# Kernel tuning notes

Hardware: AMD Instinct MI355X
Metric: run time of the kernel (lower is better)

## Reference

```python
import jax, jax.numpy as jnp
import numpy as np

TEMP = 0.07
EPS = 1e-6
NORM_EPS = 1e-12  # F.normalize default eps
LN_EPS = 1e-5

B, D, H, W = 32, 256, 64, 64
K = 256
DFF = 2048


def _l2norm(v, axis):
    n = jnp.sqrt(jnp.sum(v * v, axis=axis, keepdims=True))
    return v / jnp.maximum(n, NORM_EPS)


def _layernorm(v, g, b):
    mu = jnp.mean(v, axis=-1, keepdims=True)
    var = jnp.mean((v - mu) ** 2, axis=-1, keepdims=True)
    return (v - mu) * jax.lax.rsqrt(var + LN_EPS) * g + b


def setup_inputs() -> dict:
    key = jax.random.key(0)
    ks = jax.random.split(key, 8)
    s1 = 1.0 / np.sqrt(D)
    s2 = 1.0 / np.sqrt(DFF)
    return {
        "x": jax.random.normal(ks[0], (B, D, H, W), jnp.float32),
        "tgt": jax.random.normal(ks[1], (B, K, D), jnp.float32),
        "w1": jax.random.uniform(ks[2], (DFF, D), jnp.float32, -s1, s1),
        "b1": jax.random.uniform(ks[3], (DFF,), jnp.float32, -s1, s1),
        "w2": jax.random.uniform(ks[4], (D, DFF), jnp.float32, -s2, s2),
        "b2": jax.random.uniform(ks[5], (D,), jnp.float32, -s2, s2),
        "g2": jnp.ones((D,), jnp.float32),
        "be2": jnp.zeros((D,), jnp.float32),
        "g3": jnp.ones((D,), jnp.float32),
        "be3": jnp.zeros((D,), jnp.float32),
    }


def reference(x, tgt, w1, b1, w2, b2, g2, be2, g3, be3):
    # slot cross-attention with L2-normalized q/k
    tn = _l2norm(tgt, axis=2)           # (b,k,d)
    xn = _l2norm(x, axis=1)             # (b,d,h,w)
    dots = jnp.einsum('bkd,bdhw->bkhw', tn, xn)
    attn = jax.nn.softmax(dots / TEMP, axis=1) + EPS          # softmax over slots
    attn = attn / jnp.sum(attn, axis=(2, 3), keepdims=True)   # spatial normalization
    tgt2 = jnp.einsum('bdhw,bkhw->bkd', x, attn)
    t = _layernorm(tgt + tgt2, g2, be2)
    # FFN (dropout = identity in eval)
    ff = jnp.maximum(t @ w1.T + b1, 0.0) @ w2.T + b2
    return _layernorm(t + ff, g3, be3)
```

## Files before the change

### kernel.cpp

```cpp
#include <hip/hip_runtime.h>
#include <hip/hip_bf16.h>

using bf16 = __hip_bfloat16;

typedef __attribute__((ext_vector_type(8))) short short8;
typedef __attribute__((ext_vector_type(4))) float f32x4;

constexpr int Bb = 32, Dd = 256, HWw = 4096, Kk = 256, Ff = 2048;
constexpr float TEMP_INV = 1.0f / 0.07f;
constexpr float EPSf = 1e-6f;
constexpr float NORM_EPSf = 1e-12f;
constexpr float LN_EPSf = 1e-5f;
constexpr size_t PKD = (size_t)Bb * Kk * Dd;

static __device__ __forceinline__ float b2f(bf16 v) { return __bfloat162float(v); }
static __device__ __forceinline__ bf16 f2b(float v) { return __float2bfloat16(v); }


__global__ __launch_bounds__(64) void k_tn(const float* __restrict__ tgt,
                                           bf16* __restrict__ tnbf) {
  int row = blockIdx.x;
  int b = row >> 8, slot = row & 255;
  int lane = threadIdx.x;
  const float* src = tgt + (size_t)row * Dd + lane * 4;
  float v[4];
#pragma unroll
  for (int u = 0; u < 4; u++) v[u] = src[u];
  float ss = v[0] * v[0] + v[1] * v[1] + v[2] * v[2] + v[3] * v[3];
#pragma unroll
  for (int m = 32; m >= 1; m >>= 1) ss += __shfl_xor(ss, m, 64);
  float inv = 1.0f / fmaxf(sqrtf(ss), NORM_EPSf);
  bf16 o[4] __attribute__((aligned(8)));
#pragma unroll
  for (int u = 0; u < 4; u++) o[u] = f2b(v[u] * inv);
  int s = lane >> 3;
  int q2 = (lane >> 1) & 3;
  int jh = (lane & 1) * 4;
  size_t fi = (size_t)((slot >> 4) * 64 + q2 * 16 + (slot & 15));
  *(float2*)(tnbf + ((size_t)(b * 8 + s) * 1024 + fi) * 8 + jh) = *(float2*)o;
}

__global__ __launch_bounds__(64) void k_prew1(const float* __restrict__ w1,
                                              bf16* __restrict__ w1bf) {
  int f = blockIdx.x;
  int lane = threadIdx.x;
  const float* src = w1 + (size_t)f * Dd + lane * 4;
  bf16 o[4] __attribute__((aligned(8)));
#pragma unroll
  for (int u = 0; u < 4; u++) o[u] = f2b(src[u]);
  int s = lane >> 3;
  int q2 = (lane >> 1) & 3;
  int jh = (lane & 1) * 4;
  size_t fi = (size_t)(((f & 63) >> 4) * 64 + q2 * 16 + (f & 15));
  *(float2*)(w1bf + ((size_t)((f >> 6) * 8 + s) * 256 + fi) * 8 + jh) = *(float2*)o;
}

__global__ __launch_bounds__(64) void k_prew2(const float* __restrict__ w2,
                                              bf16* __restrict__ w2bf) {
  int d = blockIdx.x;
  int lane = threadIdx.x;
  const float* src = w2 + (size_t)d * Ff + lane * 32;
  size_t gbase = (size_t)((d >> 6) * 64 + lane) * 256;
  int fbase = ((d & 63) >> 4) * 64 + (d & 15);
#pragma unroll
  for (int q2 = 0; q2 < 4; q2++) {
    float4 v0 = *(const float4*)(src + q2 * 8);
    float4 v1 = *(const float4*)(src + q2 * 8 + 4);
    bf16 o[8] __attribute__((aligned(16)));
    o[0] = f2b(v0.x); o[1] = f2b(v0.y); o[2] = f2b(v0.z); o[3] = f2b(v0.w);
    o[4] = f2b(v1.x); o[5] = f2b(v1.y); o[6] = f2b(v1.z); o[7] = f2b(v1.w);
    *(float4*)(w2bf + (gbase + fbase + q2 * 16) * 8) = *(float4*)o;
  }
}

#define MFMA16(a, b, c) __builtin_amdgcn_mfma_f32_16x16x32_bf16(a, b, c, 0, 0, 0)

__global__ __launch_bounds__(256) void k_dots(const bf16* __restrict__ tnbf,
                                              const float* __restrict__ x,
                                              bf16* __restrict__ xb_bf,
                                              bf16* __restrict__ attn_bf,
                                              float* __restrict__ S) {
  __shared__ __align__(16) char smem[16384];
  bf16* Bs = (bf16*)smem;
  float* ssred = (float*)(smem + 8320);
  float* nxl = (float*)(smem + 12672);
  float* red = (float*)(smem + 12928);
  int b = blockIdx.x >> 6;
  int hw0 = (blockIdx.x & 63) * 64;
  int tid = threadIdx.x;
  int wave = tid >> 6, lane = tid & 63;
  int quad = lane >> 4, nl = lane & 15;

  int dp = tid >> 4;
  int ch = tid & 15;
  int qb = dp >> 2;
  int jb = (dp & 3) * 2;

  f32x4 acc[4][4];
#pragma unroll
  for (int i = 0; i < 4; i++)
#pragma unroll
    for (int j = 0; j < 4; j++) acc[i][j] = (f32x4){0.f, 0.f, 0.f, 0.f};
  float ssp[4] = {0.f, 0.f, 0.f, 0.f};

  int spx = (hw0 >> 5) + (ch >> 3);
  int q2x = (ch >> 1) & 3;
  int jx = (ch & 1) * 4;

  float4 va, vb;
  short8 afp[4];
  {
    const float* xr0 = x + (size_t)((b << 8) + 2 * dp) * HWw + hw0 + ch * 4;
    va = *(const float4*)xr0;
    vb = *(const float4*)(xr0 + HWw);
    const bf16* ts0 = tnbf + (size_t)(b * 8) * 1024 * 8;
#pragma unroll
    for (int mt = 0; mt < 4; mt++)
      afp[mt] = *(const short8*)(ts0 + (size_t)(((wave << 2) + mt) * 64 + lane) * 8);
  }

  for (int s = 0; s < 8; s++) {
    bf16* bsb = Bs + (s & 1) * 2080;
    {
      float vva[4] = {va.x, va.y, va.z, va.w};
      float vvb[4] = {vb.x, vb.y, vb.z, vb.w};
      bf16 pa[4] __attribute__((aligned(8)));
      bf16 pb[4] __attribute__((aligned(8)));
#pragma unroll
      for (int jj = 0; jj < 4; jj++) {
        ssp[jj] += vva[jj] * vva[jj] + vvb[jj] * vvb[jj];
        pa[jj] = f2b(vva[jj]);
        pb[jj] = f2b(vvb[jj]);
      }
      int d0r = s * 32 + 2 * dp;
      int fiA = (d0r >> 4) * 64 + q2x * 16 + (d0r & 15);
      size_t base = ((size_t)(b * 128) + spx) * 1024;
      *(float2*)(xb_bf + (base + fiA) * 8 + jx) = *(float2*)pa;
      *(float2*)(xb_bf + (base + fiA + 1) * 8 + jx) = *(float2*)pb;
#pragma unroll
      for (int jj = 0; jj < 4; jj++) {
        int hwl = ch * 4 + jj;
        int nt = hwl >> 4;
        int li = (qb << 4) | (hwl & 15);
        union { bf16 h[2]; unsigned int u; } pk;
        pk.h[0] = pa[jj];
        pk.h[1] = pb[jj];
        *(unsigned int*)&bsb[nt * 520 + li * 8 + jb] = pk.u;
      }
    }
    __syncthreads();
    short8 af[4];
#pragma unroll
    for (int mt = 0; mt < 4; mt++) af[mt] = afp[mt];
    if (s < 7) {
      const float* xr = x + (size_t)((b << 8) + (s + 1) * 32 + 2 * dp) * HWw + hw0 + ch * 4;
      va = *(const float4*)xr;
      vb = *(const float4*)(xr + HWw);
      const bf16* tsrc = tnbf + (size_t)(b * 8 + s + 1) * 1024 * 8;
#pragma unroll
      for (int mt = 0; mt < 4; mt++)
        afp[mt] = *(const short8*)(tsrc + (size_t)(((wave << 2) + mt) * 64 + lane) * 8);
    }
    short8 bfv[4];
#pragma unroll
    for (int nt = 0; nt < 4; nt++)
      bfv[nt] = *(const short8*)(bsb + nt * 520 + lane * 8);
#pragma unroll
    for (int mt = 0; mt < 4; mt++)
#pragma unroll
      for (int nt = 0; nt < 4; nt++) acc[mt][nt] = MFMA16(af[mt], bfv[nt], acc[mt][nt]);
  }

#pragma unroll
  for (int jj = 0; jj < 4; jj++) ssred[(ch * 4 + jj) * 17 + dp] = ssp[jj];
  __syncthreads();
  if (tid < 64) {
    float sum = 0.f;
#pragma unroll
    for (int i = 0; i < 16; i++) sum += ssred[tid * 17 + i];
    nxl[tid] = TEMP_INV / fmaxf(sqrtf(sum), NORM_EPSf);
  }
  __syncthreads();

  float sc[4];
#pragma unroll
  for (int nt = 0; nt < 4; nt++) sc[nt] = nxl[nt * 16 + nl];
#pragma unroll
  for (int mt = 0; mt < 4; mt++)
#pragma unroll
    for (int nt = 0; nt < 4; nt++)
#pragma unroll
      for (int r = 0; r < 4; r++) acc[mt][nt][r] *= sc[nt];

  float* red2 = red + 256;

  float pmax[4];
#pragma unroll
  for (int nt = 0; nt < 4; nt++) {
    float m = acc[0][nt][0];
#pragma unroll
    for (int mt = 0; mt < 4; mt++)
#pragma unroll
      for (int r = 0; r < 4; r++) m = fmaxf(m, acc[mt][nt][r]);
    m = fmaxf(m, __shfl_xor(m, 16, 64));
    m = fmaxf(m, __shfl_xor(m, 32, 64));
    pmax[nt] = m;
  }
  if (lane < 16) {
#pragma unroll
    for (int nt = 0; nt < 4; nt++) red[((wave << 2) + nt) * 16 + nl] = pmax[nt];
  }
  __syncthreads();
  float cmax[4];
#pragma unroll
  for (int nt = 0; nt < 4; nt++) {
    float m = red[nt * 16 + nl];
#pragma unroll
    for (int w2 = 1; w2 < 4; w2++) m = fmaxf(m, red[((w2 << 2) + nt) * 16 + nl]);
    cmax[nt] = m;
  }

  float psum[4];
#pragma unroll
  for (int nt = 0; nt < 4; nt++) {
    float s = 0.f;
#pragma unroll
    for (int mt = 0; mt < 4; mt++)
#pragma unroll
      for (int r = 0; r < 4; r++) {
        float e = __expf(acc[mt][nt][r] - cmax[nt]);
        acc[mt][nt][r] = e;
        s += e;
      }
    s += __shfl_xor(s, 16, 64);
    s += __shfl_xor(s, 32, 64);
    psum[nt] = s;
  }
  if (lane < 16) {
#pragma unroll
    for (int nt = 0; nt < 4; nt++) red2[((wave << 2) + nt) * 16 + nl] = psum[nt];
  }
  __syncthreads();
  float ci[4];
#pragma unroll
  for (int nt = 0; nt < 4; nt++) {
    float s = 0.f;
#pragma unroll
    for (int w2 = 0; w2 < 4; w2++) s += red2[((w2 << 2) + nt) * 16 + nl];
    ci[nt] = 1.0f / s;
  }

#pragma unroll
  for (int mt = 0; mt < 4; mt++) {
    int slotg = (b << 8) + (wave << 6) + (mt << 4) + (quad << 2);
#pragma unroll
    for (int r = 0; r < 4; r++) {
      float rs = 0.f;
#pragma unroll
      for (int nt = 0; nt < 4; nt++) {
        bf16 hb = f2b(acc[mt][nt][r] * ci[nt] + EPSf);
        float q = b2f(hb);
        acc[mt][nt][r] = q;
        rs += q;
      }
      rs += __shfl_xor(rs, 1, 64);
      rs += __shfl_xor(rs, 2, 64);
      rs += __shfl_xor(rs, 4, 64);
      rs += __shfl_xor(rs, 8, 64);
      if (nl == 0) atomicAdd(&S[slotg + r], rs);
    }
  }

  __syncthreads();
  bf16* rp = (bf16*)smem;
  int jat = nl & 7;
#pragma unroll
  for (int h = 0; h < 2; h++) {
#pragma unroll
    for (int mt = 0; mt < 4; mt++) {
      int fi0 = ((wave << 2) + mt) * 64 + (quad << 2);
#pragma unroll
      for (int ntl = 0; ntl < 2; ntl++) {
        int nt = (h << 1) + ntl;
        int q2p = (ntl << 1) + (nl >> 3);
#pragma unroll
        for (int r = 0; r < 4; r++)
          rp[(fi0 + q2p * 16 + r) * 8 + jat] = f2b(acc[mt][nt][r]);
      }
    }
    __syncthreads();
    size_t gbase = ((size_t)(b * 128) + (hw0 >> 5) + h) * 1024 * 8;
#pragma unroll
    for (int u = 0; u < 4; u++) {
      short8 vv = *(const short8*)(rp + u * 2048 + tid * 8);
      *(short8*)(attn_bf + gbase + u * 2048 + tid * 8) = vv;
    }
    if (h == 0) __syncthreads();
  }
}

__global__ __launch_bounds__(256) void k_gemm2(const bf16* __restrict__ attn_bf,
                                               const bf16* __restrict__ xb_bf,
                                               float* __restrict__ t2p) {
  int n = blockIdx.x;
  int b = n & 31;
  int r2 = n >> 5;
  int kp = r2 & 3;
  int dgrp = (r2 >> 2) & 3;
  int hs = r2 >> 4;
  int tid = threadIdx.x;
  int wave = tid >> 6, lane = tid & 63;
  int wr = wave >> 1, wc = wave & 1;

  f32x4 acc[2][2];
#pragma unroll
  for (int i = 0; i < 2; i++)
#pragma unroll
    for (int j = 0; j < 2; j++) acc[i][j] = (f32x4){0.f, 0.f, 0.f, 0.f};

  const bf16* Abase = attn_bf + ((size_t)(b * 128 + hs * 32) * 1024 + (size_t)(kp * 4 + wr * 2) * 64) * 8;
  const bf16* Bbase = xb_bf + ((size_t)(b * 128 + hs * 32) * 1024 + (size_t)(dgrp * 4 + wc * 2) * 64) * 8;
#pragma unroll 4
  for (int st = 0; st < 32; st++) {
    const bf16* Ap = Abase + (size_t)st * 1024 * 8;
    const bf16* Bp = Bbase + (size_t)st * 1024 * 8;
    short8 a0 = *(const short8*)(Ap + (size_t)lane * 8);
    short8 a1 = *(const short8*)(Ap + (size_t)(64 + lane) * 8);
    short8 b0 = *(const short8*)(Bp + (size_t)lane * 8);
    short8 b1 = *(const short8*)(Bp + (size_t)(64 + lane) * 8);
    acc[0][0] = MFMA16(a0, b0, acc[0][0]);
    acc[0][1] = MFMA16(a0, b1, acc[0][1]);
    acc[1][0] = MFMA16(a1, b0, acc[1][0]);
    acc[1][1] = MFMA16(a1, b1, acc[1][1]);
  }
  float* dst = t2p + (size_t)hs * PKD;
  int quad = lane >> 4, nl = lane & 15;
#pragma unroll
  for (int i = 0; i < 2; i++)
#pragma unroll
    for (int r = 0; r < 4; r++) {
      int row = (b << 8) + kp * 64 + wr * 32 + i * 16 + quad * 4 + r;
#pragma unroll
      for (int j = 0; j < 2; j++) {
        int col = dgrp * 64 + wc * 32 + j * 16 + nl;
        dst[(size_t)row * Dd + col] = acc[i][j][r];
      }
    }
}

__global__ __launch_bounds__(64) void k_ln_pre(const float* __restrict__ t2p,
                                               const float* __restrict__ S,
                                               const float* __restrict__ tgt,
                                               const float* __restrict__ g,
                                               const float* __restrict__ be,
                                               float* __restrict__ t,
                                               bf16* __restrict__ tbf) {
  int row = blockIdx.x;
  int lane = threadIdx.x;
  float sInv = 1.0f / S[row];
  size_t off = (size_t)row * Dd + lane * 4;
  float4 a0 = *(const float4*)(t2p + off);
  float4 a1 = *(const float4*)(t2p + PKD + off);
  float4 a2 = *(const float4*)(t2p + 2 * PKD + off);
  float4 a3 = *(const float4*)(t2p + 3 * PKD + off);
  const float* pt = tgt + off;
  float v[4];
  v[0] = (a0.x + a1.x + a2.x + a3.x) * sInv + pt[0];
  v[1] = (a0.y + a1.y + a2.y + a3.y) * sInv + pt[1];
  v[2] = (a0.z + a1.z + a2.z + a3.z) * sInv + pt[2];
  v[3] = (a0.w + a1.w + a2.w + a3.w) * sInv + pt[3];
  float s1 = v[0] + v[1] + v[2] + v[3];
  float s2 = v[0] * v[0] + v[1] * v[1] + v[2] * v[2] + v[3] * v[3];
#pragma unroll
  for (int m = 32; m >= 1; m >>= 1) {
    s1 += __shfl_xor(s1, m, 64);
    s2 += __shfl_xor(s2, m, 64);
  }
  float mu = s1 * (1.0f / 256.0f);
  float var = s2 * (1.0f / 256.0f) - mu * mu;
  float rs = rsqrtf(fmaxf(var, 0.f) + LN_EPSf);
  float* po = t + (size_t)row * Dd + lane * 4;
  bf16 o[4] __attribute__((aligned(8)));
#pragma unroll
  for (int u = 0; u < 4; u++) {
    float val = (v[u] - mu) * rs * g[lane * 4 + u] + be[lane * 4 + u];
    po[u] = val;
    o[u] = f2b(val);
  }
  int s = lane >> 3;
  int q2 = (lane >> 1) & 3;
  int jh = (lane & 1) * 4;
  size_t fi = (size_t)(((row & 63) >> 4) * 64 + q2 * 16 + (row & 15));
  *(float2*)(tbf + ((size_t)((row >> 6) * 8 + s) * 256 + fi) * 8 + jh) = *(float2*)o;
}

__global__ __launch_bounds__(256) void k_ffn1(const bf16* __restrict__ tbf,
                                              const bf16* __restrict__ w1bf,
                                              const float* __restrict__ b1,
                                              bf16* __restrict__ h1bf) {
  int rowgrp = blockIdx.x >> 5;
  int fgrp = blockIdx.x & 31;
  int tid = threadIdx.x;
  int wave = tid >> 6, lane = tid & 63;
  int am = (wave >> 1) * 2, bn = (wave & 1) * 2;

  f32x4 acc[2][2];
#pragma unroll
  for (int i = 0; i < 2; i++)
#pragma unroll
    for (int j = 0; j < 2; j++) acc[i][j] = (f32x4){0.f, 0.f, 0.f, 0.f};

  const bf16* Abase = tbf + (size_t)rowgrp * 8 * 256 * 8;
  const bf16* Bbase = w1bf + (size_t)fgrp * 8 * 256 * 8;
#pragma unroll
  for (int s = 0; s < 8; s++) {
    short8 af[2], bfr[2];
#pragma unroll
    for (int i = 0; i < 2; i++)
      af[i] = *(const short8*)(Abase + ((size_t)s * 256 + ((am + i) * 64 + lane)) * 8);
#pragma unroll
    for (int j = 0; j < 2; j++)
      bfr[j] = *(const short8*)(Bbase + ((size_t)s * 256 + ((bn + j) * 64 + lane)) * 8);
#pragma unroll
    for (int i = 0; i < 2; i++)
#pragma unroll
      for (int j = 0; j < 2; j++) acc[i][j] = MFMA16(af[i], bfr[j], acc[i][j]);
  }
  int quad = lane >> 4, nl = lane & 15;
  int jat = nl & 7;
#pragma unroll
  for (int j = 0; j < 2; j++) {
    int f = fgrp * 64 + (bn + j) * 16 + nl;
    float bias = b1[f];
    size_t sp = (size_t)(rowgrp * 64) + fgrp * 2 + ((bn + j) >> 1);
    int q2p = ((bn + j) & 1) * 2 + (nl >> 3);
#pragma unroll
    for (int i = 0; i < 2; i++) {
      int fiBase = (am + i) * 64 + q2p * 16 + (quad << 2);
#pragma unroll
      for (int r = 0; r < 4; r++) {
        float val = fmaxf(acc[i][j][r] + bias, 0.f);
        h1bf[(sp * 256 + fiBase + r) * 8 + jat] = f2b(val);
      }
    }
  }
}

__global__ __launch_bounds__(256) void k_ffn2(const bf16* __restrict__ h1bf,
                                              const bf16* __restrict__ w2bf,
                                              float* __restrict__ o2p) {
  int n = blockIdx.x;
  int rowgrp = n >> 3;
  int ksp = n & 7;
  int tid = threadIdx.x;
  int wave = tid >> 6, lane = tid & 63;

  f32x4 acc[4][4];
#pragma unroll
  for (int i = 0; i < 4; i++)
#pragma unroll
    for (int j = 0; j < 4; j++) acc[i][j] = (f32x4){0.f, 0.f, 0.f, 0.f};

#pragma unroll
  for (int st = 0; st < 8; st++) {
    int sg = ksp * 8 + st;
    const bf16* Ab = h1bf + ((size_t)(rowgrp * 64 + sg) * 256) * 8;
    const bf16* Bbv = w2bf + ((size_t)(wave * 64 + sg) * 256) * 8;
    short8 af[4], bfr[4];
#pragma unroll
    for (int mt = 0; mt < 4; mt++)
      af[mt] = *(const short8*)(Ab + (size_t)(mt * 64 + lane) * 8);
#pragma unroll
    for (int nt = 0; nt < 4; nt++)
      bfr[nt] = *(const short8*)(Bbv + (size_t)(nt * 64 + lane) * 8);
#pragma unroll
    for (int mt = 0; mt < 4; mt++)
#pragma unroll
      for (int nt = 0; nt < 4; nt++) acc[mt][nt] = MFMA16(af[mt], bfr[nt], acc[mt][nt]);
  }
  float* dst = o2p + (size_t)ksp * PKD;
  int quad = lane >> 4, nl = lane & 15;
#pragma unroll
  for (int mt = 0; mt < 4; mt++)
#pragma unroll
    for (int r = 0; r < 4; r++) {
      int row = rowgrp * 64 + mt * 16 + quad * 4 + r;
#pragma unroll
      for (int nt = 0; nt < 4; nt++) {
        int col = wave * 64 + nt * 16 + nl;
        dst[(size_t)row * Dd + col] = acc[mt][nt][r];
      }
    }
}

__global__ __launch_bounds__(64) void k_ln_out(const float* __restrict__ o2p,
                                               const float* __restrict__ b2v,
                                               const float* __restrict__ t,
                                               const float* __restrict__ g,
                                               const float* __restrict__ be,
                                               float* __restrict__ out) {
  int row = blockIdx.x;
  int lane = threadIdx.x;
  size_t off = (size_t)row * Dd + lane * 4;
  float acc4[4] = {0.f, 0.f, 0.f, 0.f};
#pragma unroll
  for (int q = 0; q < 8; q++) {
    float4 aq = *(const float4*)(o2p + (size_t)q * PKD + off);
    acc4[0] += aq.x;
    acc4[1] += aq.y;
    acc4[2] += aq.z;
    acc4[3] += aq.w;
  }
  const float* pt = t + off;
  float v[4];
#pragma unroll
  for (int u = 0; u < 4; u++) v[u] = acc4[u] + b2v[lane * 4 + u] + pt[u];
  float s1 = v[0] + v[1] + v[2] + v[3];
  float s2 = v[0] * v[0] + v[1] * v[1] + v[2] * v[2] + v[3] * v[3];
#pragma unroll
  for (int m = 32; m >= 1; m >>= 1) {
    s1 += __shfl_xor(s1, m, 64);
    s2 += __shfl_xor(s2, m, 64);
  }
  float mu = s1 * (1.0f / 256.0f);
  float var = s2 * (1.0f / 256.0f) - mu * mu;
  float rs = rsqrtf(fmaxf(var, 0.f) + LN_EPSf);
  float* pw = out + (size_t)row * Dd + lane * 4;
#pragma unroll
  for (int u = 0; u < 4; u++)
    pw[u] = (v[u] - mu) * rs * g[lane * 4 + u] + be[lane * 4 + u];
}

extern "C" void kernel_launch(void* const* d_in, const int* in_sizes, int n_in,
                              void* d_out, int out_size, void* d_ws, size_t ws_size,
                              hipStream_t stream) {
  const float* x = (const float*)d_in[0];
  const float* tgt = (const float*)d_in[1];
  const float* w1 = (const float*)d_in[2];
  const float* b1 = (const float*)d_in[3];
  const float* w2 = (const float*)d_in[4];
  const float* b2v = (const float*)d_in[5];
  const float* g2 = (const float*)d_in[6];
  const float* be2 = (const float*)d_in[7];
  const float* g3 = (const float*)d_in[8];
  const float* be3 = (const float*)d_in[9];
  float* out = (float*)d_out;

  char* w = (char*)d_ws;
  bf16* tnbf = (bf16*)w;     w += (size_t)Bb * Kk * Dd * 2;
  float* S = (float*)w;      w += (size_t)Bb * Kk * 4;
  float* t = (float*)w;      w += (size_t)Bb * Kk * Dd * 4;
  bf16* attn_bf = (bf16*)w;  w += (size_t)Bb * HWw * Kk * 2;
  bf16* h1bf = (bf16*)w;     w += (size_t)Bb * Kk * Ff * 2;
  bf16* xb_bf = (bf16*)w;    w += (size_t)Bb * Dd * HWw * 2;

  bf16* tbf = tnbf;
  bf16* w1bf = attn_bf;
  bf16* w2bf = attn_bf + (size_t)Ff * Dd;
  float* t2p = (float*)h1bf;
  float* o2p = (float*)xb_bf;

  hipMemsetAsync(S, 0, (size_t)Bb * Kk * 4, stream);
  k_tn<<<Bb * Kk, 64, 0, stream>>>(tgt, tnbf);
  k_dots<<<Bb * (HWw / 64), 256, 0, stream>>>(tnbf, x, xb_bf, attn_bf, S);
  k_gemm2<<<2048, 256, 0, stream>>>(attn_bf, xb_bf, t2p);
  k_prew1<<<Ff, 64, 0, stream>>>(w1, w1bf);
  k_prew2<<<Dd, 64, 0, stream>>>(w2, w2bf);
  k_ln_pre<<<Bb * Kk, 64, 0, stream>>>(t2p, S, tgt, g2, be2, t, tbf);
  k_ffn1<<<(Bb * Kk / 64) * (Ff / 64), 256, 0, stream>>>(tbf, w1bf, b1, h1bf);
  k_ffn2<<<(Bb * Kk / 64) * 8, 256, 0, stream>>>(h1bf, w2bf, o2p);
  k_ln_out<<<Bb * Kk, 64, 0, stream>>>(o2p, b2v, t, g3, be3, out);
}
```

Baseline: 411.0 us.

## Remove split-K partial buffers, swizzle staged stores, move xb_bf store past barrier

k_gemm2 stops splitting the spatial reduction into four partial outputs and instead loops over the whole 4096 range per block. k_ffn2 now reduces its K-split across waves in shared memory rather than writing eight global partials. Both LN kernels therefore read a single buffer. k_dots and k_ffn1 stage their bf16 outputs through LDS with an XOR swizzle so global writes are coalesced, and the xb_bf global store in k_dots now happens after the barrier. The aim is to cut global partial-sum traffic and scattered stores, at the cost of fewer blocks (less parallelism) in gemm2 and ffn2 and more shared memory in ffn2.

```diff
diff --git a/kernel.cpp b/kernel.cpp
--- a/kernel.cpp
+++ b/kernel.cpp
@@ -11,7 +11,6 @@
 constexpr float EPSf = 1e-6f;
 constexpr float NORM_EPSf = 1e-12f;
 constexpr float LN_EPSf = 1e-5f;
-constexpr size_t PKD = (size_t)Bb * Kk * Dd;
 
 static __device__ __forceinline__ float b2f(bf16 v) { return __bfloat162float(v); }
 static __device__ __forceinline__ bf16 f2b(float v) { return __float2bfloat16(v); }
@@ -121,22 +120,17 @@
 
   for (int s = 0; s < 8; s++) {
     bf16* bsb = Bs + (s & 1) * 2080;
+    bf16 pa[4] __attribute__((aligned(8)));
+    bf16 pb[4] __attribute__((aligned(8)));
     {
       float vva[4] = {va.x, va.y, va.z, va.w};
       float vvb[4] = {vb.x, vb.y, vb.z, vb.w};
-      bf16 pa[4] __attribute__((aligned(8)));
-      bf16 pb[4] __attribute__((aligned(8)));
 #pragma unroll
       for (int jj = 0; jj < 4; jj++) {
         ssp[jj] += vva[jj] * vva[jj] + vvb[jj] * vvb[jj];
         pa[jj] = f2b(vva[jj]);
         pb[jj] = f2b(vvb[jj]);
       }
-      int d0r = s * 32 + 2 * dp;
-      int fiA = (d0r >> 4) * 64 + q2x * 16 + (d0r & 15);
-      size_t base = ((size_t)(b * 128) + spx) * 1024;
-      *(float2*)(xb_bf + (base + fiA) * 8 + jx) = *(float2*)pa;
-      *(float2*)(xb_bf + (base + fiA + 1) * 8 + jx) = *(float2*)pb;
 #pragma unroll
       for (int jj = 0; jj < 4; jj++) {
         int hwl = ch * 4 + jj;
@@ -148,10 +142,17 @@
         *(unsigned int*)&bsb[nt * 520 + li * 8 + jb] = pk.u;
       }
     }
+    short8 af[4];
+#pragma unroll
+    for (int mt = 0; mt < 4; mt++) af[mt] = afp[mt];
     __syncthreads();
-    short8 af[4];
-#pragma unroll
-    for (int mt = 0; mt < 4; mt++) af[mt] = afp[mt];
+    {
+      int d0r = s * 32 + 2 * dp;
+      int fiA = (d0r >> 4) * 64 + q2x * 16 + (d0r & 15);
+      size_t base = ((size_t)(b * 128) + spx) * 1024;
+      *(float2*)(xb_bf + (base + fiA) * 8 + jx) = *(float2*)pa;
+      *(float2*)(xb_bf + (base + fiA + 1) * 8 + jx) = *(float2*)pb;
+    }
     if (s < 7) {
       const float* xr = x + (size_t)((b << 8) + (s + 1) * 32 + 2 * dp) * HWw + hw0 + ch * 4;
       va = *(const float4*)xr;
@@ -284,16 +285,21 @@
         int nt = (h << 1) + ntl;
         int q2p = (ntl << 1) + (nl >> 3);
 #pragma unroll
-        for (int r = 0; r < 4; r++)
-          rp[(fi0 + q2p * 16 + r) * 8 + jat] = f2b(acc[mt][nt][r]);
+        for (int r = 0; r < 4; r++) {
+          int fi = fi0 + q2p * 16 + r;
+          int fisw = fi ^ ((fi >> 3) & 3);
+          rp[fisw * 8 + jat] = f2b(acc[mt][nt][r]);
+        }
       }
     }
     __syncthreads();
     size_t gbase = ((size_t)(b * 128) + (hw0 >> 5) + h) * 1024 * 8;
 #pragma unroll
     for (int u = 0; u < 4; u++) {
-      short8 vv = *(const short8*)(rp + u * 2048 + tid * 8);
-      *(short8*)(attn_bf + gbase + u * 2048 + tid * 8) = vv;
+      int fl = u * 256 + tid;
+      int fg = fl ^ ((fl >> 3) & 3);
+      short8 vv = *(const short8*)(rp + (size_t)fl * 8);
+      *(short8*)(attn_bf + gbase + (size_t)fg * 8) = vv;
     }
     if (h == 0) __syncthreads();
   }
@@ -301,13 +307,12 @@
 
 __global__ __launch_bounds__(256) void k_gemm2(const bf16* __restrict__ attn_bf,
                                                const bf16* __restrict__ xb_bf,
-                                               float* __restrict__ t2p) {
+                                               float* __restrict__ t2) {
   int n = blockIdx.x;
   int b = n & 31;
   int r2 = n >> 5;
   int kp = r2 & 3;
-  int dgrp = (r2 >> 2) & 3;
-  int hs = r2 >> 4;
+  int dgrp = r2 >> 2;
   int tid = threadIdx.x;
   int wave = tid >> 6, lane = tid & 63;
   int wr = wave >> 1, wc = wave & 1;
@@ -318,10 +323,10 @@
 #pragma unroll
     for (int j = 0; j < 2; j++) acc[i][j] = (f32x4){0.f, 0.f, 0.f, 0.f};
 
-  const bf16* Abase = attn_bf + ((size_t)(b * 128 + hs * 32) * 1024 + (size_t)(kp * 4 + wr * 2) * 64) * 8;
-  const bf16* Bbase = xb_bf + ((size_t)(b * 128 + hs * 32) * 1024 + (size_t)(dgrp * 4 + wc * 2) * 64) * 8;
+  const bf16* Abase = attn_bf + ((size_t)(b * 128) * 1024 + (size_t)(kp * 4 + wr * 2) * 64) * 8;
+  const bf16* Bbase = xb_bf + ((size_t)(b * 128) * 1024 + (size_t)(dgrp * 4 + wc * 2) * 64) * 8;
 #pragma unroll 4
-  for (int st = 0; st < 32; st++) {
+  for (int st = 0; st < 128; st++) {
     const bf16* Ap = Abase + (size_t)st * 1024 * 8;
     const bf16* Bp = Bbase + (size_t)st * 1024 * 8;
     short8 a0 = *(const short8*)(Ap + (size_t)lane * 8);
@@ -333,7 +338,6 @@
     acc[1][0] = MFMA16(a1, b0, acc[1][0]);
     acc[1][1] = MFMA16(a1, b1, acc[1][1]);
   }
-  float* dst = t2p + (size_t)hs * PKD;
   int quad = lane >> 4, nl = lane & 15;
 #pragma unroll
   for (int i = 0; i < 2; i++)
@@ -343,12 +347,12 @@
 #pragma unroll
       for (int j = 0; j < 2; j++) {
         int col = dgrp * 64 + wc * 32 + j * 16 + nl;
-        dst[(size_t)row * Dd + col] = acc[i][j][r];
-      }
-    }
-}
-
-__global__ __launch_bounds__(64) void k_ln_pre(const float* __restrict__ t2p,
+        t2[(size_t)row * Dd + col] = acc[i][j][r];
+      }
+    }
+}
+
+__global__ __launch_bounds__(64) void k_ln_pre(const float* __restrict__ t2,
                                                const float* __restrict__ S,
                                                const float* __restrict__ tgt,
                                                const float* __restrict__ g,
@@ -359,16 +363,13 @@
   int lane = threadIdx.x;
   float sInv = 1.0f / S[row];
   size_t off = (size_t)row * Dd + lane * 4;
-  float4 a0 = *(const float4*)(t2p + off);
-  float4 a1 = *(const float4*)(t2p + PKD + off);
-  float4 a2 = *(const float4*)(t2p + 2 * PKD + off);
-  float4 a3 = *(const float4*)(t2p + 3 * PKD + off);
+  float4 a0 = *(const float4*)(t2 + off);
   const float* pt = tgt + off;
   float v[4];
-  v[0] = (a0.x + a1.x + a2.x + a3.x) * sInv + pt[0];
-  v[1] = (a0.y + a1.y + a2.y + a3.y) * sInv + pt[1];
-  v[2] = (a0.z + a1.z + a2.z + a3.z) * sInv + pt[2];
-  v[3] = (a0.w + a1.w + a2.w + a3.w) * sInv + pt[3];
+  v[0] = a0.x * sInv + pt[0];
+  v[1] = a0.y * sInv + pt[1];
+  v[2] = a0.z * sInv + pt[2];
+  v[3] = a0.w * sInv + pt[3];
   float s1 = v[0] + v[1] + v[2] + v[3];
   float s2 = v[0] * v[0] + v[1] * v[1] + v[2] * v[2] + v[3] * v[3];
 #pragma unroll
@@ -398,6 +399,7 @@
                                               const bf16* __restrict__ w1bf,
                                               const float* __restrict__ b1,
                                               bf16* __restrict__ h1bf) {
+  __shared__ __align__(16) bf16 rp[512 * 8];
   int rowgrp = blockIdx.x >> 5;
   int fgrp = blockIdx.x & 31;
   int tid = threadIdx.x;
@@ -432,7 +434,7 @@
   for (int j = 0; j < 2; j++) {
     int f = fgrp * 64 + (bn + j) * 16 + nl;
     float bias = b1[f];
-    size_t sp = (size_t)(rowgrp * 64) + fgrp * 2 + ((bn + j) >> 1);
+    int seth = (bn + j) >> 1;
     int q2p = ((bn + j) & 1) * 2 + (nl >> 3);
 #pragma unroll
     for (int i = 0; i < 2; i++) {
@@ -440,18 +442,30 @@
 #pragma unroll
       for (int r = 0; r < 4; r++) {
         float val = fmaxf(acc[i][j][r] + bias, 0.f);
-        h1bf[(sp * 256 + fiBase + r) * 8 + jat] = f2b(val);
-      }
-    }
+        int fi = fiBase + r;
+        int fisw = fi ^ ((fi >> 3) & 3);
+        rp[(seth * 256 + fisw) * 8 + jat] = f2b(val);
+      }
+    }
+  }
+  __syncthreads();
+  size_t sp0 = (size_t)(rowgrp * 64) + fgrp * 2;
+#pragma unroll
+  for (int u = 0; u < 2; u++) {
+    int loc = tid;
+    int fg = loc ^ ((loc >> 3) & 3);
+    short8 vv = *(const short8*)(rp + ((size_t)u * 256 + loc) * 8);
+    *(short8*)(h1bf + ((sp0 + u) * 256 + fg) * 8) = vv;
   }
 }
 
 __global__ __launch_bounds__(256) void k_ffn2(const bf16* __restrict__ h1bf,
                                               const bf16* __restrict__ w2bf,
-                                              float* __restrict__ o2p) {
+                                              float* __restrict__ o2) {
+  __shared__ float redsm[4 * 4160];
   int n = blockIdx.x;
-  int rowgrp = n >> 3;
-  int ksp = n & 7;
+  int rowgrp = n >> 2;
+  int cg = n & 3;
   int tid = threadIdx.x;
   int wave = tid >> 6, lane = tid & 63;
 
@@ -461,11 +475,11 @@
 #pragma unroll
     for (int j = 0; j < 4; j++) acc[i][j] = (f32x4){0.f, 0.f, 0.f, 0.f};
 
-#pragma unroll
-  for (int st = 0; st < 8; st++) {
-    int sg = ksp * 8 + st;
+#pragma unroll 4
+  for (int stl = 0; stl < 16; stl++) {
+    int sg = wave * 16 + stl;
     const bf16* Ab = h1bf + ((size_t)(rowgrp * 64 + sg) * 256) * 8;
-    const bf16* Bbv = w2bf + ((size_t)(wave * 64 + sg) * 256) * 8;
+    const bf16* Bbv = w2bf + ((size_t)(cg * 64 + sg) * 256) * 8;
     short8 af[4], bfr[4];
 #pragma unroll
     for (int mt = 0; mt < 4; mt++)
@@ -478,22 +492,29 @@
 #pragma unroll
       for (int nt = 0; nt < 4; nt++) acc[mt][nt] = MFMA16(af[mt], bfr[nt], acc[mt][nt]);
   }
-  float* dst = o2p + (size_t)ksp * PKD;
   int quad = lane >> 4, nl = lane & 15;
+  float* my = redsm + wave * 4160;
 #pragma unroll
   for (int mt = 0; mt < 4; mt++)
 #pragma unroll
     for (int r = 0; r < 4; r++) {
-      int row = rowgrp * 64 + mt * 16 + quad * 4 + r;
-#pragma unroll
-      for (int nt = 0; nt < 4; nt++) {
-        int col = wave * 64 + nt * 16 + nl;
-        dst[(size_t)row * Dd + col] = acc[mt][nt][r];
-      }
-    }
-}
-
-__global__ __launch_bounds__(64) void k_ln_out(const float* __restrict__ o2p,
+      int row = mt * 16 + quad * 4 + r;
+#pragma unroll
+      for (int nt = 0; nt < 4; nt++)
+        my[row * 65 + nt * 16 + nl] = acc[mt][nt][r];
+    }
+  __syncthreads();
+#pragma unroll
+  for (int u = 0; u < 16; u++) {
+    int o = u * 256 + tid;
+    int row = o >> 6, col = o & 63;
+    int li = row * 65 + col;
+    float ssum = redsm[li] + redsm[4160 + li] + redsm[8320 + li] + redsm[12480 + li];
+    o2[(size_t)(rowgrp * 64 + row) * Dd + cg * 64 + col] = ssum;
+  }
+}
+
+__global__ __launch_bounds__(64) void k_ln_out(const float* __restrict__ o2,
                                                const float* __restrict__ b2v,
                                                const float* __restrict__ t,
                                                const float* __restrict__ g,
@@ -502,19 +523,13 @@
   int row = blockIdx.x;
   int lane = threadIdx.x;
   size_t off = (size_t)row * Dd + lane * 4;
-  float acc4[4] = {0.f, 0.f, 0.f, 0.f};
-#pragma unroll
-  for (int q = 0; q < 8; q++) {
-    float4 aq = *(const float4*)(o2p + (size_t)q * PKD + off);
-    acc4[0] += aq.x;
-    acc4[1] += aq.y;
-    acc4[2] += aq.z;
-    acc4[3] += aq.w;
-  }
+  float4 aq = *(const float4*)(o2 + off);
   const float* pt = t + off;
   float v[4];
-#pragma unroll
-  for (int u = 0; u < 4; u++) v[u] = acc4[u] + b2v[lane * 4 + u] + pt[u];
+  v[0] = aq.x + b2v[lane * 4 + 0] + pt[0];
+  v[1] = aq.y + b2v[lane * 4 + 1] + pt[1];
+  v[2] = aq.z + b2v[lane * 4 + 2] + pt[2];
+  v[3] = aq.w + b2v[lane * 4 + 3] + pt[3];
   float s1 = v[0] + v[1] + v[2] + v[3];
   float s2 = v[0] * v[0] + v[1] * v[1] + v[2] * v[2] + v[3] * v[3];
 #pragma unroll
@@ -557,17 +572,17 @@
   bf16* tbf = tnbf;
   bf16* w1bf = attn_bf;
   bf16* w2bf = attn_bf + (size_t)Ff * Dd;
-  float* t2p = (float*)h1bf;
-  float* o2p = (float*)xb_bf;
+  float* t2 = (float*)h1bf;
+  float* o2 = (float*)xb_bf;
 
   hipMemsetAsync(S, 0, (size_t)Bb * Kk * 4, stream);
   k_tn<<<Bb * Kk, 64, 0, stream>>>(tgt, tnbf);
   k_dots<<<Bb * (HWw / 64), 256, 0, stream>>>(tnbf, x, xb_bf, attn_bf, S);
-  k_gemm2<<<2048, 256, 0, stream>>>(attn_bf, xb_bf, t2p);
+  k_gemm2<<<512, 256, 0, stream>>>(attn_bf, xb_bf, t2);
   k_prew1<<<Ff, 64, 0, stream>>>(w1, w1bf);
   k_prew2<<<Dd, 64, 0, stream>>>(w2, w2bf);
-  k_ln_pre<<<Bb * Kk, 64, 0, stream>>>(t2p, S, tgt, g2, be2, t, tbf);
+  k_ln_pre<<<Bb * Kk, 64, 0, stream>>>(t2, S, tgt, g2, be2, t, tbf);
   k_ffn1<<<(Bb * Kk / 64) * (Ff / 64), 256, 0, stream>>>(tbf, w1bf, b1, h1bf);
-  k_ffn2<<<(Bb * Kk / 64) * 8, 256, 0, stream>>>(h1bf, w2bf, o2p);
-  k_ln_out<<<Bb * Kk, 64, 0, stream>>>(o2p, b2v, t, g3, be3, out);
-}
+  k_ffn2<<<512, 256, 0, stream>>>(h1bf, w2bf, o2);
+  k_ln_out<<<Bb * Kk, 64, 0, stream>>>(o2, b2v, t, g3, be3, out);
+}
```

Result: no change. 407.7 us (-0.8%).
